# Kernel tuning notes

Hardware: AMD Instinct MI355X
Metric: run time of the kernel (lower is better)

The kernel has to match this reference:

```python
import math
import jax, jax.numpy as jnp
import numpy as np

B, S, E, H, P = 8, 1024, 512, 8, 32
MAXD, OFFS, LW, STL, HID = 256, 8.0, 4, 4, 2048

def _lin(x, w, b):
    return x @ w.T + b

def _gelu(x):
    return jax.nn.gelu(x, approximate=False)  # torch nn.GELU default (erf)

def _ln(x, g, b, eps=1e-5):
    m = x.mean(-1, keepdims=True)
    v = ((x - m) ** 2).mean(-1, keepdims=True)
    return (x - m) / jnp.sqrt(v + eps) * g + b

def setup_inputs() -> dict:
    key = jax.random.key(0)
    ks = iter(jax.random.split(key, 40))
    def w(*shape):
        return (jax.random.normal(next(ks), shape, dtype=jnp.float32) * 0.02)
    x = jax.random.normal(next(ks), (B, S, E), dtype=jnp.float32)
    lengths = jax.random.randint(next(ks), (B,), S // 2, S + 1)
    padding_mask = jnp.arange(S)[None, :] >= lengths[:, None]  # (B,S) bool
    inp = dict(x=x, padding_mask=padding_mask)
    # local MHA (torch nn.MultiheadAttention packed in_proj)
    inp.update(in_proj_w=w(3 * E, E), in_proj_b=jnp.zeros((3 * E,), jnp.float32),
               mha_out_w=w(E, E), mha_out_b=jnp.zeros((E,), jnp.float32))
    # deformable attention projections
    for nm in ('dq', 'dk', 'dv', 'do'):
        inp[nm + '_w'] = w(E, E); inp[nm + '_b'] = jnp.zeros((E,), jnp.float32)
    inp.update(off1_w=w(E, E), off1_b=jnp.zeros((E,), jnp.float32),
               off2_w=w(H * P, E), off2_b=jnp.zeros((H * P,), jnp.float32))
    inp.update(gate1_w=w(E, 3 * E), gate1_b=jnp.zeros((E,), jnp.float32),
               gate2_w=w(E, E), gate2_b=jnp.zeros((E,), jnp.float32))
    inp.update(n1_g=jnp.ones((E,), jnp.float32), n1_b=jnp.zeros((E,), jnp.float32),
               n2_g=jnp.ones((E,), jnp.float32), n2_b=jnp.zeros((E,), jnp.float32))
    inp.update(ffn1_w=w(HID, E), ffn1_b=jnp.zeros((HID,), jnp.float32),
               ffn2_w=w(E, HID), ffn2_b=jnp.zeros((E,), jnp.float32))
    return inp

def _forward(x, padding_mask, in_proj_w, in_proj_b, mha_out_w, mha_out_b,
             dq_w, dq_b, dk_w, dk_b, dv_w, dv_b, do_w, do_b,
             off1_w, off1_b, off2_w, off2_b, gate1_w, gate1_b, gate2_w, gate2_b,
             n1_g, n1_b, n2_g, n2_b, ffn1_w, ffn1_b, ffn2_w, ffn2_b):
    Bv, Sv, Ev = x.shape
    hd = Ev // H
    pos = jnp.arange(Sv)
    # ---------------- local causal windowed MHA ----------------
    qkv = _lin(x, in_proj_w, in_proj_b)
    q, k, v = jnp.split(qkv, 3, axis=-1)
    q = q.reshape(Bv, Sv, H, hd).transpose(0, 2, 1, 3)  # bhsd
    k = k.reshape(Bv, Sv, H, hd).transpose(0, 2, 1, 3)
    v = v.reshape(Bv, Sv, H, hd).transpose(0, 2, 1, 3)
    scores = jnp.einsum('bhqd,bhkd->bhqk', q, k) / math.sqrt(hd)
    future = pos[None, :] > pos[:, None]
    too_far = (pos[:, None] - pos[None, :]) >= min(LW, STL)
    lmask = (future | too_far)[None, None] | padding_mask[:, None, None, :]
    scores = jnp.where(lmask, -jnp.inf, scores)
    allm = lmask.all(-1, keepdims=True)
    scores = jnp.where(allm, 0.0, scores)  # avoid NaN on fully-masked (padded) rows
    attn = jax.nn.softmax(scores, axis=-1)
    attn = jnp.where(lmask, 0.0, attn)
    lo = jnp.einsum('bhqk,bhkd->bhqd', attn, v).transpose(0, 2, 1, 3).reshape(Bv, Sv, Ev)
    local_out = _lin(lo, mha_out_w, mha_out_b)
    # ---------------- deformable long-history attention ----------------
    anchors = jnp.linspace(0.1, 0.9, P)
    valid_len = jnp.clip(Sv - padding_mask.sum(-1), 1, None)
    positions = pos[None, :, None].astype(jnp.float32)  # (1,S,1)
    base = anchors[None, None, :] * positions
    off = jnp.tanh(_lin(_gelu(_lin(x, off1_w, off1_b)), off2_w, off2_b))
    off = off.reshape(Bv, Sv, H, P).mean(2) * OFFS
    sampled = base + off
    sampled = jnp.clip(sampled, jnp.clip(positions - MAXD, 0, None), positions)
    sampled = jnp.minimum(sampled, (valid_len - 1).astype(jnp.float32)[:, None, None])
    sp = jnp.round(sampled).astype(jnp.int32)  # (B,S,P) sample positions
    qd = _lin(x, dq_w, dq_b)
    kd = _lin(x, dk_w, dk_b)
    vd = _lin(x, dv_w, dv_b)
    bidx = jnp.arange(Bv)[:, None, None]
    k_sp = kd[bidx, sp]  # (B,S,P,E) gathered keys
    v_sp = vd[bidx, sp]
    sc = jnp.einsum('bqd,bqpd->bqp', qd, k_sp) / math.sqrt(Ev)
    samp_inv = padding_mask[bidx, sp]
    causal_inv = sp > pos[None, :, None]
    rb = jnp.clip(pos[:, None] - (STL - 1), 0, None)
    long_mem_mask = pos[None, :] >= rb  # (S,S): forbid recent short-term positions
    extra_inv = long_mem_mask[pos[None, :, None], sp]
    inv = samp_inv | causal_inv | extra_inv
    sc = jnp.where(inv, -jnp.inf, sc)
    alli = inv.all(-1, keepdims=True)
    sc = jnp.where(alli, 0.0, sc)
    a = jax.nn.softmax(sc, axis=-1)
    a = jnp.where(inv, 0.0, a)
    long_out = _lin(jnp.einsum('bqp,bqpd->bqd', a, v_sp), do_w, do_b)
    # ---------------- gate fuse + FFN ----------------
    cat = jnp.concatenate([x, local_out, long_out], axis=-1)
    g = jax.nn.sigmoid(_lin(_gelu(_lin(cat, gate1_w, gate1_b)), gate2_w, gate2_b))
    fused = g * local_out + (1.0 - g) * long_out
    x1 = _ln(x + fused, n1_g, n1_b)
    f = _lin(_gelu(_lin(x1, ffn1_w, ffn1_b)), ffn2_w, ffn2_b)
    return _ln(x1 + f, n2_g, n2_b)

def reference(x, padding_mask, in_proj_w, in_proj_b, mha_out_w, mha_out_b,
              dq_w, dq_b, dk_w, dk_b, dv_w, dv_b, do_w, do_b,
              off1_w, off1_b, off2_w, off2_b, gate1_w, gate1_b, gate2_w, gate2_b,
              n1_g, n1_b, n2_g, n2_b, ffn1_w, ffn1_b, ffn2_w, ffn2_b):
    return _forward(x, padding_mask, in_proj_w, in_proj_b, mha_out_w, mha_out_b,
                    dq_w, dq_b, dk_w, dk_b, dv_w, dv_b, do_w, do_b,
                    off1_w, off1_b, off2_w, off2_b, gate1_w, gate1_b, gate2_w, gate2_b,
                    n1_g, n1_b, n2_g, n2_b, ffn1_w, ffn1_b, ffn2_w, ffn2_b)
```

## Files before the change

kernel.cpp:

```cpp
#include <hip/hip_runtime.h>
#include <hip/hip_bf16.h>
#include <type_traits>

typedef __hip_bfloat16 bf16;
typedef __attribute__((ext_vector_type(8))) short short8;
typedef __attribute__((ext_vector_type(4))) float floatx4;

static constexpr int kB = 8;
static constexpr int kS = 1024;
static constexpr int kE = 512;
static constexpr int kH = 8;
static constexpr int kP = 32;
static constexpr int kTok = kB * kS;
static constexpr int kHid = 2048;

__device__ __forceinline__ void load8f(const bf16* p, float* f) {
  uint4 u = *(const uint4*)p;
  const bf16* h = (const bf16*)&u;
#pragma unroll
  for (int e = 0; e < 8; e++) f[e] = __bfloat162float(h[e]);
}
__device__ __forceinline__ void store8b(bf16* p, const float* f) {
  uint4 u;
  bf16* h = (bf16*)&u;
#pragma unroll
  for (int e = 0; e < 8; e++) h[e] = __float2bfloat16(f[e]);
  *(uint4*)p = u;
}
__device__ __forceinline__ bool is_pad(const void* pm, int flag, int idx) {
  return flag ? (((const int*)pm)[idx] != 0)
              : (((const unsigned char*)pm)[idx] != 0);
}
__device__ __forceinline__ float fast_gelu(float x) {
  float u = x * (0.7978845608f + 0.044714998f * x * x);
  float e = __expf(2.0f * u);
  float t = 1.0f - 2.0f / (e + 1.0f);
  return 0.5f * x * (1.0f + t);
}
__device__ __forceinline__ void dma16(const bf16* g, bf16* l) {
  __builtin_amdgcn_global_load_lds(
      (const __attribute__((address_space(1))) unsigned int*)g,
      (__attribute__((address_space(3))) unsigned int*)l, 16, 0, 0);
}

__global__ __launch_bounds__(256) void detect_kernel(const void* __restrict__ x,
                                                     int* __restrict__ meta) {
  __shared__ int cnt;
  if (threadIdx.x == 0) cnt = 0;
  __syncthreads();
  const unsigned short* u = (const unsigned short*)x;
  int c = 0;
  for (int i = threadIdx.x; i < 1024; i += 256) {
    int e = (u[i] >> 7) & 0xFF;
    if (e >= 0x90) c++;
  }
  if (c) atomicAdd(&cnt, c);
  __syncthreads();
  if (threadIdx.x == 0) meta[9] = (cnt > 64) ? 1 : 0;
}

__global__ __launch_bounds__(256) void meta_kernel(const void* __restrict__ pm,
                                                   int* __restrict__ meta) {
  __shared__ int bigfound;
  __shared__ int cnt[kB];
  int tid = threadIdx.x;
  if (tid == 0) bigfound = 0;
  if (tid < kB) cnt[tid] = 0;
  __syncthreads();
  const unsigned int* w = (const unsigned int*)pm;
  int f = 0;
  for (int i = tid; i < 2048; i += 256)
    if (w[i] & 0xFFFFFFFEu) f = 1;
  if (f) atomicOr(&bigfound, 1);
  __syncthreads();
  int flag = bigfound ? 0 : 1;
  for (int i = tid; i < kTok; i += 256) {
    if (is_pad(pm, flag, i)) atomicAdd(&cnt[i >> 10], 1);
  }
  __syncthreads();
  if (tid == 0) meta[0] = flag;
  if (tid < kB) {
    int vl = kS - cnt[tid];
    if (vl < 1) vl = 1;
    meta[1 + tid] = vl;
  }
}

struct CvtJob { const void* src; bf16* hi; bf16* lo; int nblk; };
struct CvtJobs { CvtJob j[13]; };
__global__ __launch_bounds__(256) void cvt_all_kernel(CvtJobs jobs,
                                                      const int* __restrict__ meta) {
  int fp = meta[9];
  int b = blockIdx.x, ji = 0;
  while (b >= jobs.j[ji].nblk) { b -= jobs.j[ji].nblk; ji++; }
  CvtJob J = jobs.j[ji];
  int i = b * 1024 + threadIdx.x * 4;
  float v[4];
  if (fp) {
    float4 f = ((const float4*)J.src)[i >> 2];
    v[0] = f.x; v[1] = f.y; v[2] = f.z; v[3] = f.w;
  } else {
    uint2 u = *(const uint2*)((const bf16*)J.src + i);
    const bf16* h = (const bf16*)&u;
#pragma unroll
    for (int e = 0; e < 4; e++) v[e] = __bfloat162float(h[e]);
  }
  uint2 uh;
  bf16* hh = (bf16*)&uh;
#pragma unroll
  for (int e = 0; e < 4; e++) hh[e] = __float2bfloat16(v[e]);
  *(uint2*)(J.hi + i) = uh;
  if (J.lo) {
    uint2 ul;
    bf16* hl = (bf16*)&ul;
#pragma unroll
    for (int e = 0; e < 4; e++)
      hl[e] = __float2bfloat16(v[e] - __bfloat162float(hh[e]));
    *(uint2*)(J.lo + i) = ul;
  }
}

struct CvtFJob { const void* src; float* dst; int n; };
struct CvtFJobs { CvtFJob j[16]; };
__global__ __launch_bounds__(256) void cvt_small_kernel(CvtFJobs jobs,
                                                        const int* __restrict__ meta) {
  int fp = meta[9];
#pragma unroll 1
  for (int ji = 0; ji < 16; ji++) {
    CvtFJob J = jobs.j[ji];
    for (int i = threadIdx.x; i < J.n; i += 256)
      J.dst[i] = fp ? ((const float*)J.src)[i]
                    : __bfloat162float(((const bf16*)J.src)[i]);
  }
}

static constexpr int BK = 32;

template <int BM, int BN, int ACT, typename OUTT>
__device__ __forceinline__ void gemm_core(const bf16* __restrict__ A,
                                          const bf16* __restrict__ W,
                                          const float* __restrict__ bias,
                                          OUTT* __restrict__ C, int N, int K,
                                          int m0, int n0) {
  constexpr int WR = (BM == 128 && BN == 128) ? 4 : 2;
  constexpr int WC = 4;
  __shared__ bf16 As[BM * BK];
  __shared__ bf16 Bs[BN * BK];
  const int tid = threadIdx.x;
  const int lane = tid & 63;
  const int wid = tid >> 6;
  int wm, wn;
  if constexpr (BM == 128 && BN == 128) {
    wm = (wid >> 1) * 64; wn = (wid & 1) * 64;
  } else {
    wm = wid * 32; wn = 0;
  }

  floatx4 acc[WR][WC];
#pragma unroll
  for (int i = 0; i < WR; i++)
#pragma unroll
    for (int j = 0; j < WC; j++) acc[i][j] = (floatx4)0.0f;

  for (int kt = 0; kt < K; kt += BK) {
#pragma unroll
    for (int c = 0; c < BM / 64; c++) {
      int seg = c * 64 + wid * 16;
      int row = seg + (lane >> 2);
      int ch = (lane & 3) ^ ((row >> 1) & 3);
      dma16(&A[(size_t)(m0 + row) * K + kt + ch * 8], &As[seg * BK]);
    }
#pragma unroll
    for (int c = 0; c < BN / 64; c++) {
      int seg = c * 64 + wid * 16;
      int row = seg + (lane >> 2);
      int ch = (lane & 3) ^ ((row >> 1) & 3);
      dma16(&W[(size_t)(n0 + row) * K + kt + ch * 8], &Bs[seg * BK]);
    }
    __syncthreads();
    const int kb = lane >> 4;
    short8 af[WR], bfr[WC];
#pragma unroll
    for (int i = 0; i < WR; i++) {
      int r = wm + i * 16 + (lane & 15);
      af[i] = *(const short8*)(&As[r * BK + ((kb ^ ((r >> 1) & 3)) << 3)]);
    }
#pragma unroll
    for (int j = 0; j < WC; j++) {
      int r = wn + j * 16 + (lane & 15);
      bfr[j] = *(const short8*)(&Bs[r * BK + ((kb ^ ((r >> 1) & 3)) << 3)]);
    }
#pragma unroll
    for (int i = 0; i < WR; i++)
#pragma unroll
      for (int j = 0; j < WC; j++)
        acc[i][j] = __builtin_amdgcn_mfma_f32_16x16x32_bf16(bfr[j], af[i],
                                                            acc[i][j], 0, 0, 0);
    __syncthreads();
  }

#pragma unroll
  for (int i = 0; i < WR; i++) {
    int row = m0 + wm + i * 16 + (lane & 15);
#pragma unroll
    for (int j = 0; j < WC; j++) {
      int col = n0 + wn + j * 16 + ((lane >> 4) << 2);
      float bv[4] = {0.f, 0.f, 0.f, 0.f};
      if (bias) {
        float4 b4 = *(const float4*)&bias[col];
        bv[0] = b4.x; bv[1] = b4.y; bv[2] = b4.z; bv[3] = b4.w;
      }
      float v[4];
#pragma unroll
      for (int r = 0; r < 4; r++) {
        v[r] = acc[i][j][r] + bv[r];
        if (ACT == 1) v[r] = fast_gelu(v[r]);
        else if (ACT == 2) v[r] = 1.0f / (1.0f + __expf(-v[r]));
      }
      size_t idx = (size_t)row * N + col;
      if constexpr (std::is_same<OUTT, float>::value) {
        *(float4*)&C[idx] = make_float4(v[0], v[1], v[2], v[3]);
      } else {
        uint2 u;
        bf16* h = (bf16*)&u;
#pragma unroll
        for (int r = 0; r < 4; r++) h[r] = __float2bfloat16(v[r]);
        *(uint2*)&C[idx] = u;
      }
    }
  }
}

template <int BM, int BN, int ACT, typename OUTT>
__global__ __launch_bounds__(256) void gemm_bt(
    const bf16* __restrict__ A, const bf16* __restrict__ W,
    const float* __restrict__ bias, OUTT* __restrict__ C, int N, int K) {
  gemm_core<BM, BN, ACT, OUTT>(A, W, bias, C, N, K, blockIdx.x * BM,
                               blockIdx.y * BN);
}

__global__ __launch_bounds__(256) void gemm_pair(
    const bf16* __restrict__ A0, const bf16* __restrict__ W0,
    const float* __restrict__ b0, bf16* __restrict__ C0,
    const bf16* __restrict__ A1, const bf16* __restrict__ W1,
    const float* __restrict__ b1, bf16* __restrict__ C1, int N, int K) {
  int nb = N >> 6;
  bool s = (int)blockIdx.y >= nb;
  gemm_core<128, 64, 0, bf16>(s ? A1 : A0, s ? W1 : W0, s ? b1 : b0,
                              s ? C1 : C0, N, K, blockIdx.x * 128,
                              (s ? (int)blockIdx.y - nb : (int)blockIdx.y) * 64);
}

__global__ __launch_bounds__(256) void gemm_gate1(
    const bf16* __restrict__ x, const bf16* __restrict__ lo,
    const bf16* __restrict__ lg, const bf16* __restrict__ W,
    const float* __restrict__ bias, bf16* __restrict__ C) {
  constexpr int BM = 128, BN = 64, WR = 2, WC = 4;
  constexpr int N = 512, K = 1536;
  __shared__ bf16 As[BM * BK];
  __shared__ bf16 Bs[BN * BK];
  const int tid = threadIdx.x;
  const int lane = tid & 63;
  const int wid = tid >> 6;
  const int wm = wid * 32, wn = 0;
  const int m0 = blockIdx.x * BM, n0 = blockIdx.y * BN;

  floatx4 acc[WR][WC];
#pragma unroll
  for (int i = 0; i < WR; i++)
#pragma unroll
    for (int j = 0; j < WC; j++) acc[i][j] = (floatx4)0.0f;

  for (int kt = 0; kt < K; kt += BK) {
    const bf16* src = (kt < 512) ? x : (kt < 1024) ? lo : lg;
    int kk = kt & 511;
#pragma unroll
    for (int c = 0; c < 2; c++) {
      int seg = c * 64 + wid * 16;
      int row = seg + (lane >> 2);
      int ch = (lane & 3) ^ ((row >> 1) & 3);
      dma16(&src[(size_t)(m0 + row) * 512 + kk + ch * 8], &As[seg * BK]);
    }
    {
      int seg = wid * 16;
      int row = seg + (lane >> 2);
      int ch = (lane & 3) ^ ((row >> 1) & 3);
      dma16(&W[(size_t)(n0 + row) * K + kt + ch * 8], &Bs[seg * BK]);
    }
    __syncthreads();
    const int kb = lane >> 4;
    short8 af[WR], bfr[WC];
#pragma unroll
    for (int i = 0; i < WR; i++) {
      int r = wm + i * 16 + (lane & 15);
      af[i] = *(const short8*)(&As[r * BK + ((kb ^ ((r >> 1) & 3)) << 3)]);
    }
#pragma unroll
    for (int j = 0; j < WC; j++) {
      int r = wn + j * 16 + (lane & 15);
      bfr[j] = *(const short8*)(&Bs[r * BK + ((kb ^ ((r >> 1) & 3)) << 3)]);
    }
#pragma unroll
    for (int i = 0; i < WR; i++)
#pragma unroll
      for (int j = 0; j < WC; j++)
        acc[i][j] = __builtin_amdgcn_mfma_f32_16x16x32_bf16(bfr[j], af[i],
                                                            acc[i][j], 0, 0, 0);
    __syncthreads();
  }

#pragma unroll
  for (int i = 0; i < WR; i++) {
    int row = m0 + wm + i * 16 + (lane & 15);
#pragma unroll
    for (int j = 0; j < WC; j++) {
      int col = n0 + wn + j * 16 + ((lane >> 4) << 2);
      float4 b4 = *(const float4*)&bias[col];
      float bv[4] = {b4.x, b4.y, b4.z, b4.w};
      uint2 u;
      bf16* h = (bf16*)&u;
#pragma unroll
      for (int r = 0; r < 4; r++)
        h[r] = __float2bfloat16(fast_gelu(acc[i][j][r] + bv[r]));
      *(uint2*)&C[(size_t)row * N + col] = u;
    }
  }
}

template <int BM, int BN, bool SPLIT>
__global__ __launch_bounds__(256) void gemm3_bt(
    const bf16* __restrict__ Ah, const bf16* __restrict__ Al,
    const bf16* __restrict__ Wh, const bf16* __restrict__ Wl,
    const float* __restrict__ bias, float* __restrict__ Cf,
    bf16* __restrict__ Chi, bf16* __restrict__ Clo, int N, int K) {
  constexpr int WR = 2;
  constexpr int WC = (BM == 128) ? 4 : 2;
  __shared__ bf16 Ash[BM * BK];
  __shared__ bf16 Asl[BM * BK];
  __shared__ bf16 Bsh[BN * BK];
  __shared__ bf16 Bsl[BN * BK];
  const int tid = threadIdx.x;
  const int lane = tid & 63;
  const int wid = tid >> 6;
  int wm, wn;
  if constexpr (BM == 128) {
    wm = wid * 32; wn = 0;
  } else {
    wm = (wid >> 1) * 32; wn = (wid & 1) * 32;
  }
  const int m0 = blockIdx.x * BM, n0 = blockIdx.y * BN;

  floatx4 acc[WR][WC];
#pragma unroll
  for (int i = 0; i < WR; i++)
#pragma unroll
    for (int j = 0; j < WC; j++) acc[i][j] = (floatx4)0.0f;

  for (int kt = 0; kt < K; kt += BK) {
#pragma unroll
    for (int c = 0; c < BM / 64; c++) {
      int seg = c * 64 + wid * 16;
      int row = seg + (lane >> 2);
      int ch = (lane & 3) ^ ((row >> 1) & 3);
      size_t g = (size_t)(m0 + row) * K + kt + ch * 8;
      dma16(&Ah[g], &Ash[seg * BK]);
      dma16(&Al[g], &Asl[seg * BK]);
    }
#pragma unroll
    for (int c = 0; c < BN / 64; c++) {
      int seg = c * 64 + wid * 16;
      int row = seg + (lane >> 2);
      int ch = (lane & 3) ^ ((row >> 1) & 3);
      size_t g = (size_t)(n0 + row) * K + kt + ch * 8;
      dma16(&Wh[g], &Bsh[seg * BK]);
      dma16(&Wl[g], &Bsl[seg * BK]);
    }
    __syncthreads();
    const int kb = lane >> 4;
    short8 ah[WR], al[WR], bh[WC], bl[WC];
#pragma unroll
    for (int i = 0; i < WR; i++) {
      int r = wm + i * 16 + (lane & 15);
      int ro = r * BK + ((kb ^ ((r >> 1) & 3)) << 3);
      ah[i] = *(const short8*)(&Ash[ro]);
      al[i] = *(const short8*)(&Asl[ro]);
    }
#pragma unroll
    for (int j = 0; j < WC; j++) {
      int r = wn + j * 16 + (lane & 15);
      int ro = r * BK + ((kb ^ ((r >> 1) & 3)) << 3);
      bh[j] = *(const short8*)(&Bsh[ro]);
      bl[j] = *(const short8*)(&Bsl[ro]);
    }
#pragma unroll
    for (int i = 0; i < WR; i++)
#pragma unroll
      for (int j = 0; j < WC; j++) {
        acc[i][j] = __builtin_amdgcn_mfma_f32_16x16x32_bf16(bh[j], ah[i],
                                                            acc[i][j], 0, 0, 0);
        acc[i][j] = __builtin_amdgcn_mfma_f32_16x16x32_bf16(bl[j], ah[i],
                                                            acc[i][j], 0, 0, 0);
        acc[i][j] = __builtin_amdgcn_mfma_f32_16x16x32_bf16(bh[j], al[i],
                                                            acc[i][j], 0, 0, 0);
      }
    __syncthreads();
  }

#pragma unroll
  for (int i = 0; i < WR; i++) {
    int row = m0 + wm + i * 16 + (lane & 15);
#pragma unroll
    for (int j = 0; j < WC; j++) {
      int col = n0 + wn + j * 16 + ((lane >> 4) << 2);
      float4 b4 = *(const float4*)&bias[col];
      float bv[4] = {b4.x, b4.y, b4.z, b4.w};
      if constexpr (SPLIT) {
        uint2 uh, ul;
        bf16* hh = (bf16*)&uh;
        bf16* hl = (bf16*)&ul;
#pragma unroll
        for (int r = 0; r < 4; r++) {
          float v = acc[i][j][r] + bv[r];
          float g = 0.5f * v * (1.0f + erff(v * 0.70710678118654752f));
          bf16 hi = __float2bfloat16(g);
          hh[r] = hi;
          hl[r] = __float2bfloat16(g - __bfloat162float(hi));
        }
        *(uint2*)&Chi[(size_t)row * N + col] = uh;
        *(uint2*)&Clo[(size_t)row * N + col] = ul;
      } else {
        *(float4*)&Cf[(size_t)row * N + col] =
            make_float4(acc[i][j][0] + bv[0], acc[i][j][1] + bv[1],
                        acc[i][j][2] + bv[2], acc[i][j][3] + bv[3]);
      }
    }
  }
}

__global__ __launch_bounds__(256) void local_attn_kernel(
    const bf16* __restrict__ qkv, const void* __restrict__ pm,
    const int* __restrict__ meta, bf16* __restrict__ lo) {
  int lane = threadIdx.x & 63;
  int t = blockIdx.x * 4 + (threadIdx.x >> 6);
  int b = t >> 10, s = t & 1023;
  int h = lane >> 3, sub = lane & 7;
  int flag = meta[0];
  float q[8];
  load8f(qkv + (size_t)t * 3072 + h * 64 + sub * 8, q);
  float sc[4];
  bool val[4];
#pragma unroll
  for (int w = 0; w < 4; w++) {
    int kp = s - 3 + w;
    bool v = (kp >= 0) && !is_pad(pm, flag, b * kS + kp);
    float d = 0.0f;
    if (v) {
      float kk[8];
      load8f(qkv + (size_t)(b * kS + kp) * 3072 + 512 + h * 64 + sub * 8, kk);
#pragma unroll
      for (int e = 0; e < 8; e++) d += q[e] * kk[e];
    }
    d += __shfl_xor(d, 1);
    d += __shfl_xor(d, 2);
    d += __shfl_xor(d, 4);
    sc[w] = v ? d / 8.0f : -INFINITY;
    val[w] = v;
  }
  float mx = fmaxf(fmaxf(sc[0], sc[1]), fmaxf(sc[2], sc[3]));
  float a[4] = {0.f, 0.f, 0.f, 0.f};
  if (mx != -INFINITY) {
    float ssum = 0.f;
#pragma unroll
    for (int w = 0; w < 4; w++) {
      float e = val[w] ? expf(sc[w] - mx) : 0.0f;
      a[w] = e;
      ssum += e;
    }
#pragma unroll
    for (int w = 0; w < 4; w++) a[w] /= ssum;
  }
  float o[8] = {0.f, 0.f, 0.f, 0.f, 0.f, 0.f, 0.f, 0.f};
#pragma unroll
  for (int w = 0; w < 4; w++) {
    if (val[w] && a[w] > 0.0f) {
      int kp = s - 3 + w;
      float vv[8];
      load8f(qkv + (size_t)(b * kS + kp) * 3072 + 1024 + h * 64 + sub * 8, vv);
#pragma unroll
      for (int e = 0; e < 8; e++) o[e] += a[w] * vv[e];
    }
  }
  store8b(lo + (size_t)t * kE + lane * 8, o);
}

__global__ __launch_bounds__(256) void sampler_kernel(
    const float* __restrict__ rawf, const void* __restrict__ pm,
    const int* __restrict__ meta, int* __restrict__ sp,
    unsigned int* __restrict__ invm) {
  int t = blockIdx.x * 8 + (threadIdx.x >> 5);
  int p = threadIdx.x & 31;
  int b = t >> 10, s = t & 1023;
  int flag = meta[0];
  float off = 0.0f;
#pragma unroll
  for (int h = 0; h < kH; h++) off += tanhf(rawf[(size_t)t * 256 + h * kP + p]);
  double anchor = 0.1 + 0.8 * (double)p / 31.0;
  double sampled = anchor * (double)s + (double)off;
  double lov = fmax(0.0, (double)s - 256.0);
  sampled = fmin(fmax(sampled, lov), (double)s);
  int vlen = meta[1 + b];
  sampled = fmin(sampled, (double)(vlen - 1));
  int spv = (int)rint(sampled);
  bool inv = is_pad(pm, flag, b * kS + spv) || (spv > s) ||
             (spv >= max(0, s - 3));
  sp[(size_t)t * kP + p] = spv;
  unsigned long long m = __ballot(inv);
  int lane = threadIdx.x & 63;
  if (lane == 0) invm[t] = (unsigned int)m;
  if (lane == 32) invm[t] = (unsigned int)(m >> 32);
}

__global__ __launch_bounds__(256) void long_attn_kernel(
    const bf16* __restrict__ qkv, const int* __restrict__ sp,
    const unsigned int* __restrict__ invm, bf16* __restrict__ ctx) {
  int lane = threadIdx.x & 63;
  int bid = blockIdx.x;
  int sbid = (bid & 7) * 256 + (bid >> 3);
  int t = sbid * 4 + (threadIdx.x >> 6);
  int b = t >> 10;
  int p = lane & 31;
  int row_abs = b * kS + sp[(size_t)t * kP + p];
  float q[8];
  load8f(qkv + (size_t)t * 3072 + 1536 + lane * 8, q);
  float sc_mine = 0.0f;
#pragma unroll 4
  for (int pp = 0; pp < 32; pp++) {
    int row = __shfl(row_abs, pp);
    float kk[8];
    load8f(qkv + (size_t)row * 3072 + 2048 + lane * 8, kk);
    float d = 0.0f;
#pragma unroll
    for (int e = 0; e < 8; e++) d += q[e] * kk[e];
#pragma unroll
    for (int m = 1; m < 64; m <<= 1) d += __shfl_xor(d, m);
    if (p == pp) sc_mine = d;
  }
  bool inv = (invm[t] >> p) & 1u;
  float sc = inv ? -INFINITY : sc_mine / 22.627416997969522f;
  float mx = sc;
#pragma unroll
  for (int m = 1; m < 32; m <<= 1) mx = fmaxf(mx, __shfl_xor(mx, m));
  float e = (inv || mx == -INFINITY) ? 0.0f : expf(sc - mx);
  float ssum = e;
#pragma unroll
  for (int m = 1; m < 32; m <<= 1) ssum += __shfl_xor(ssum, m);
  float a = (ssum > 0.0f) ? e / ssum : 0.0f;
  float o[8] = {0.f, 0.f, 0.f, 0.f, 0.f, 0.f, 0.f, 0.f};
#pragma unroll 4
  for (int pp = 0; pp < 32; pp++) {
    float ap = __shfl(a, pp);
    int row = __shfl(row_abs, pp);
    if (ap != 0.0f) {
      float vv[8];
      load8f(qkv + (size_t)row * 3072 + 2560 + lane * 8, vv);
#pragma unroll
      for (int e2 = 0; e2 < 8; e2++) o[e2] += ap * vv[e2];
    }
  }
  store8b(ctx + (size_t)t * kE + lane * 8, o);
}

__global__ __launch_bounds__(256) void ln1_kernel(
    const void* __restrict__ xin, const int* __restrict__ meta,
    const bf16* __restrict__ lo, const bf16* __restrict__ lg,
    const bf16* __restrict__ g, const float* __restrict__ gamma,
    const float* __restrict__ beta, bf16* __restrict__ x1b,
    float* __restrict__ x1f) {
  int lane = threadIdx.x & 63;
  int t = blockIdx.x * 4 + (threadIdx.x >> 6);
  size_t base = (size_t)t * kE + lane * 8;
  float xv[8], lov[8], lgv[8], gv[8], h[8];
  if (meta[9]) {
    const float4* xf = (const float4*)((const float*)xin + base);
    float4 a = xf[0], b2 = xf[1];
    xv[0] = a.x; xv[1] = a.y; xv[2] = a.z; xv[3] = a.w;
    xv[4] = b2.x; xv[5] = b2.y; xv[6] = b2.z; xv[7] = b2.w;
  } else {
    load8f((const bf16*)xin + base, xv);
  }
  load8f(lo + base, lov);
  load8f(lg + base, lgv);
  load8f(g + base, gv);
  float s1 = 0.f, s2 = 0.f;
#pragma unroll
  for (int e = 0; e < 8; e++) {
    h[e] = xv[e] + gv[e] * lov[e] + (1.0f - gv[e]) * lgv[e];
    s1 += h[e];
    s2 += h[e] * h[e];
  }
#pragma unroll
  for (int m = 1; m < 64; m <<= 1) {
    s1 += __shfl_xor(s1, m);
    s2 += __shfl_xor(s2, m);
  }
  float mean = s1 * (1.0f / kE);
  float var = s2 * (1.0f / kE) - mean * mean;
  float rstd = 1.0f / sqrtf(var + 1e-5f);
  float y[8];
#pragma unroll
  for (int e = 0; e < 8; e++)
    y[e] = (h[e] - mean) * rstd * gamma[lane * 8 + e] + beta[lane * 8 + e];
  store8b(x1b + base, y);
#pragma unroll
  for (int e = 0; e < 8; e++) x1f[base + e] = y[e];
}

__global__ __launch_bounds__(256) void ln2_kernel(
    const float* __restrict__ x1f, const float* __restrict__ ff,
    const float* __restrict__ gamma, const float* __restrict__ beta,
    const int* __restrict__ meta, void* __restrict__ out) {
  int lane = threadIdx.x & 63;
  int t = blockIdx.x * 4 + (threadIdx.x >> 6);
  size_t base = (size_t)t * kE + lane * 8;
  float h[8];
  float s1 = 0.f, s2 = 0.f;
#pragma unroll
  for (int e = 0; e < 8; e++) {
    h[e] = x1f[base + e] + ff[base + e];
    s1 += h[e];
    s2 += h[e] * h[e];
  }
#pragma unroll
  for (int m = 1; m < 64; m <<= 1) {
    s1 += __shfl_xor(s1, m);
    s2 += __shfl_xor(s2, m);
  }
  float mean = s1 * (1.0f / kE);
  float var = s2 * (1.0f / kE) - mean * mean;
  float rstd = 1.0f / sqrtf(var + 1e-5f);
  float y[8];
#pragma unroll
  for (int e = 0; e < 8; e++)
    y[e] = (h[e] - mean) * rstd * gamma[lane * 8 + e] + beta[lane * 8 + e];
  if (meta[9]) {
    float* of = (float*)out + base;
    ((float4*)of)[0] = make_float4(y[0], y[1], y[2], y[3]);
    ((float4*)of)[1] = make_float4(y[4], y[5], y[6], y[7]);
  } else {
    store8b((bf16*)out + base, y);
  }
}

extern "C" void kernel_launch(void* const* d_in, const int* in_sizes, int n_in,
                              void* d_out, int out_size, void* d_ws,
                              size_t ws_size, hipStream_t stream) {
  const void* x = d_in[0];
  const void* pm = d_in[1];

  char* w = (char*)d_ws;
  auto alloc = [&](size_t bytes) {
    char* p = w;
    w += (bytes + 255) & ~(size_t)255;
    return p;
  };
  bf16* qkv_all = (bf16*)alloc((size_t)kTok * 3072 * 2);
  bf16* lo_ctx = (bf16*)alloc((size_t)kTok * kE * 2);
  bf16* ctx2 = (bf16*)alloc((size_t)kTok * kE * 2);
  bf16* local_out = (bf16*)alloc((size_t)kTok * kE * 2);
  bf16* long_out = (bf16*)alloc((size_t)kTok * kE * 2);
  bf16* hbuf = (bf16*)alloc((size_t)kTok * kE * 2);
  bf16* gbuf = (bf16*)alloc((size_t)kTok * kE * 2);
  bf16* x1b = (bf16*)alloc((size_t)kTok * kE * 2);
  float* x1f = (float*)alloc((size_t)kTok * kE * 4);
  float* rawf = (float*)alloc((size_t)kTok * 256 * 4);
  int* sp = (int*)alloc((size_t)kTok * kP * 4);
  unsigned int* invm = (unsigned int*)alloc((size_t)kTok * 4);
  int* meta = (int*)alloc(256);
  bf16* x_hi = (bf16*)alloc((size_t)kTok * kE * 2);
  bf16* x_lo = (bf16*)alloc((size_t)kTok * kE * 2);
  bf16* wall = (bf16*)alloc((size_t)3072 * 512 * 2);
  bf16* mow = (bf16*)alloc(512 * 512 * 2);
  bf16* dow = (bf16*)alloc(512 * 512 * 2);
  bf16* o1h = (bf16*)alloc(512 * 512 * 2);
  bf16* o1l = (bf16*)alloc(512 * 512 * 2);
  bf16* o2h = (bf16*)alloc(256 * 512 * 2);
  bf16* o2l = (bf16*)alloc(256 * 512 * 2);
  bf16* g1w = (bf16*)alloc(512 * 1536 * 2);
  bf16* g2w = (bf16*)alloc(512 * 512 * 2);
  bf16* f1w = (bf16*)alloc((size_t)2048 * 512 * 2);
  bf16* f2w = (bf16*)alloc((size_t)512 * 2048 * 2);
  float* ball = (float*)alloc(3072 * 4);
  float* mob = (float*)alloc(512 * 4);
  float* dob = (float*)alloc(512 * 4);
  float* o1b = (float*)alloc(512 * 4);
  float* o2b = (float*)alloc(256 * 4);
  float* g1b = (float*)alloc(512 * 4);
  float* g2b = (float*)alloc(512 * 4);
  float* n1g = (float*)alloc(512 * 4);
  float* n1bt = (float*)alloc(512 * 4);
  float* n2g = (float*)alloc(512 * 4);
  float* n2bt = (float*)alloc(512 * 4);
  float* f1b = (float*)alloc(2048 * 4);
  float* f2b = (float*)alloc(512 * 4);

  bf16* h_hi = hbuf;
  bf16* h_lo = x1b;
  float* f_f32 = (float*)qkv_all;
  bf16* ffn_h = (bf16*)((char*)qkv_all + (size_t)kTok * kE * 4);

  dim3 blk(256);
  detect_kernel<<<1, blk, 0, stream>>>(x, meta);
  meta_kernel<<<1, blk, 0, stream>>>(pm, meta);

  CvtJobs J;
  auto job = [](const void* s, bf16* hi, bf16* lo, int n) {
    CvtJob j; j.src = s; j.hi = hi; j.lo = lo; j.nblk = n >> 10; return j;
  };
  J.j[0] = job(d_in[0], x_hi, x_lo, kTok * kE);
  J.j[1] = job(d_in[2], wall, nullptr, 1536 * 512);
  J.j[2] = job(d_in[6], wall + (size_t)1536 * 512, nullptr, 512 * 512);
  J.j[3] = job(d_in[8], wall + (size_t)2048 * 512, nullptr, 512 * 512);
  J.j[4] = job(d_in[10], wall + (size_t)2560 * 512, nullptr, 512 * 512);
  J.j[5] = job(d_in[4], mow, nullptr, 512 * 512);
  J.j[6] = job(d_in[12], dow, nullptr, 512 * 512);
  J.j[7] = job(d_in[14], o1h, o1l, 512 * 512);
  J.j[8] = job(d_in[16], o2h, o2l, 256 * 512);
  J.j[9] = job(d_in[18], g1w, nullptr, 512 * 1536);
  J.j[10] = job(d_in[20], g2w, nullptr, 512 * 512);
  J.j[11] = job(d_in[26], f1w, nullptr, 2048 * 512);
  J.j[12] = job(d_in[28], f2w, nullptr, 512 * 2048);
  int totblk = 0;
  for (int i = 0; i < 13; i++) totblk += J.j[i].nblk;
  cvt_all_kernel<<<totblk, blk, 0, stream>>>(J, meta);

  CvtFJobs JF;
  auto fjob = [](const void* s, float* d, int n) {
    CvtFJob j; j.src = s; j.dst = d; j.n = n; return j;
  };
  JF.j[0] = fjob(d_in[3], ball, 1536);
  JF.j[1] = fjob(d_in[7], ball + 1536, 512);
  JF.j[2] = fjob(d_in[9], ball + 2048, 512);
  JF.j[3] = fjob(d_in[11], ball + 2560, 512);
  JF.j[4] = fjob(d_in[5], mob, 512);
  JF.j[5] = fjob(d_in[13], dob, 512);
  JF.j[6] = fjob(d_in[15], o1b, 512);
  JF.j[7] = fjob(d_in[17], o2b, 256);
  JF.j[8] = fjob(d_in[19], g1b, 512);
  JF.j[9] = fjob(d_in[21], g2b, 512);
  JF.j[10] = fjob(d_in[22], n1g, 512);
  JF.j[11] = fjob(d_in[23], n1bt, 512);
  JF.j[12] = fjob(d_in[24], n2g, 512);
  JF.j[13] = fjob(d_in[25], n2bt, 512);
  JF.j[14] = fjob(d_in[27], f1b, 2048);
  JF.j[15] = fjob(d_in[29], f2b, 512);
  cvt_small_kernel<<<1, blk, 0, stream>>>(JF, meta);

  gemm_bt<128, 128, 0, bf16><<<dim3(64, 24), blk, 0, stream>>>(
      x_hi, wall, ball, qkv_all, 3072, kE);
  gemm3_bt<128, 64, true><<<dim3(64, 8), blk, 0, stream>>>(
      x_hi, x_lo, o1h, o1l, o1b, nullptr, h_hi, h_lo, kE, kE);
  local_attn_kernel<<<2048, blk, 0, stream>>>(qkv_all, pm, meta, lo_ctx);
  gemm3_bt<64, 64, false><<<dim3(128, 4), blk, 0, stream>>>(
      h_hi, h_lo, o2h, o2l, o2b, rawf, nullptr, nullptr, 256, kE);
  sampler_kernel<<<1024, blk, 0, stream>>>(rawf, pm, meta, sp, invm);
  long_attn_kernel<<<2048, blk, 0, stream>>>(qkv_all, sp, invm, ctx2);

  gemm_pair<<<dim3(64, 16), blk, 0, stream>>>(lo_ctx, mow, mob, local_out,
                                              ctx2, dow, dob, long_out, kE, kE);

  gemm_gate1<<<dim3(64, 8), blk, 0, stream>>>(x_hi, local_out, long_out, g1w,
                                              g1b, hbuf);
  gemm_bt<128, 64, 2, bf16><<<dim3(64, 8), blk, 0, stream>>>(
      hbuf, g2w, g2b, gbuf, kE, kE);

  ln1_kernel<<<2048, blk, 0, stream>>>(x, meta, local_out, long_out, gbuf, n1g,
                                       n1bt, x1b, x1f);
  gemm_bt<128, 128, 1, bf16><<<dim3(64, 16), blk, 0, stream>>>(
      x1b, f1w, f1b, ffn_h, kHid, kE);
  gemm_bt<128, 64, 0, float><<<dim3(64, 8), blk, 0, stream>>>(
      ffn_h, f2w, f2b, f_f32, kE, kHid);
  ln2_kernel<<<2048, blk, 0, stream>>>(x1f, f_f32, n2g, n2bt, meta, d_out);
}
```

Baseline: 477.1 us.

## Double-buffer GEMM LDS tiles and skip low-part MFMAs for bf16 inputs

The bf16 GEMM cores (gemm_core and gemm_gate1) now use two LDS buffers, so the next K tile's global-to-LDS DMA is issued before the current tile's MFMAs run. Explicit waitcnt drains keep this correct. The split-precision gemm3_bt now reads the detected input-format flag and skips loading the low-part weight and activation tiles, and their extra MFMAs, when inputs are not fp32. The aim is to hide load latency and cut redundant compensation work. This doubles LDS use per block, which may reduce occupancy, and the full waitcnt drain each iteration may limit how much overlap is actually achieved.

```diff
diff --git a/kernel.cpp b/kernel.cpp
--- a/kernel.cpp
+++ b/kernel.cpp
@@ -42,6 +42,7 @@
       (const __attribute__((address_space(1))) unsigned int*)g,
       (__attribute__((address_space(3))) unsigned int*)l, 16, 0, 0);
 }
+__device__ __forceinline__ void drain_all() { __builtin_amdgcn_s_waitcnt(0); }
 
 __global__ __launch_bounds__(256) void detect_kernel(const void* __restrict__ x,
                                                      int* __restrict__ meta) {
@@ -144,8 +145,8 @@
                                           int m0, int n0) {
   constexpr int WR = (BM == 128 && BN == 128) ? 4 : 2;
   constexpr int WC = 4;
-  __shared__ bf16 As[BM * BK];
-  __shared__ bf16 Bs[BN * BK];
+  __shared__ bf16 As[2][BM * BK];
+  __shared__ bf16 Bs[2][BN * BK];
   const int tid = threadIdx.x;
   const int lane = tid & 63;
   const int wid = tid >> 6;
@@ -156,39 +157,47 @@
     wm = wid * 32; wn = 0;
   }
 
-  floatx4 acc[WR][WC];
-#pragma unroll
-  for (int i = 0; i < WR; i++)
-#pragma unroll
-    for (int j = 0; j < WC; j++) acc[i][j] = (floatx4)0.0f;
-
-  for (int kt = 0; kt < K; kt += BK) {
+  auto stage = [&](int buf, int kt) {
 #pragma unroll
     for (int c = 0; c < BM / 64; c++) {
       int seg = c * 64 + wid * 16;
       int row = seg + (lane >> 2);
       int ch = (lane & 3) ^ ((row >> 1) & 3);
-      dma16(&A[(size_t)(m0 + row) * K + kt + ch * 8], &As[seg * BK]);
+      dma16(&A[(size_t)(m0 + row) * K + kt + ch * 8], &As[buf][seg * BK]);
     }
 #pragma unroll
     for (int c = 0; c < BN / 64; c++) {
       int seg = c * 64 + wid * 16;
       int row = seg + (lane >> 2);
       int ch = (lane & 3) ^ ((row >> 1) & 3);
-      dma16(&W[(size_t)(n0 + row) * K + kt + ch * 8], &Bs[seg * BK]);
-    }
-    __syncthreads();
+      dma16(&W[(size_t)(n0 + row) * K + kt + ch * 8], &Bs[buf][seg * BK]);
+    }
+  };
+
+  floatx4 acc[WR][WC];
+#pragma unroll
+  for (int i = 0; i < WR; i++)
+#pragma unroll
+    for (int j = 0; j < WC; j++) acc[i][j] = (floatx4)0.0f;
+
+  stage(0, 0);
+  drain_all();
+  __syncthreads();
+  const int niter = K / BK;
+  for (int k = 0; k < niter; k++) {
+    const int cur = k & 1;
+    if (k + 1 < niter) stage(cur ^ 1, (k + 1) * BK);
     const int kb = lane >> 4;
     short8 af[WR], bfr[WC];
 #pragma unroll
     for (int i = 0; i < WR; i++) {
       int r = wm + i * 16 + (lane & 15);
-      af[i] = *(const short8*)(&As[r * BK + ((kb ^ ((r >> 1) & 3)) << 3)]);
+      af[i] = *(const short8*)(&As[cur][r * BK + ((kb ^ ((r >> 1) & 3)) << 3)]);
     }
 #pragma unroll
     for (int j = 0; j < WC; j++) {
       int r = wn + j * 16 + (lane & 15);
-      bfr[j] = *(const short8*)(&Bs[r * BK + ((kb ^ ((r >> 1) & 3)) << 3)]);
+      bfr[j] = *(const short8*)(&Bs[cur][r * BK + ((kb ^ ((r >> 1) & 3)) << 3)]);
     }
 #pragma unroll
     for (int i = 0; i < WR; i++)
@@ -196,6 +205,7 @@
       for (int j = 0; j < WC; j++)
         acc[i][j] = __builtin_amdgcn_mfma_f32_16x16x32_bf16(bfr[j], af[i],
                                                             acc[i][j], 0, 0, 0);
+    drain_all();
     __syncthreads();
   }
 
@@ -257,21 +267,15 @@
     const float* __restrict__ bias, bf16* __restrict__ C) {
   constexpr int BM = 128, BN = 64, WR = 2, WC = 4;
   constexpr int N = 512, K = 1536;
-  __shared__ bf16 As[BM * BK];
-  __shared__ bf16 Bs[BN * BK];
+  __shared__ bf16 As[2][BM * BK];
+  __shared__ bf16 Bs[2][BN * BK];
   const int tid = threadIdx.x;
   const int lane = tid & 63;
   const int wid = tid >> 6;
   const int wm = wid * 32, wn = 0;
   const int m0 = blockIdx.x * BM, n0 = blockIdx.y * BN;
 
-  floatx4 acc[WR][WC];
-#pragma unroll
-  for (int i = 0; i < WR; i++)
-#pragma unroll
-    for (int j = 0; j < WC; j++) acc[i][j] = (floatx4)0.0f;
-
-  for (int kt = 0; kt < K; kt += BK) {
+  auto stage = [&](int buf, int kt) {
     const bf16* src = (kt < 512) ? x : (kt < 1024) ? lo : lg;
     int kk = kt & 511;
 #pragma unroll
@@ -279,26 +283,40 @@
       int seg = c * 64 + wid * 16;
       int row = seg + (lane >> 2);
       int ch = (lane & 3) ^ ((row >> 1) & 3);
-      dma16(&src[(size_t)(m0 + row) * 512 + kk + ch * 8], &As[seg * BK]);
+      dma16(&src[(size_t)(m0 + row) * 512 + kk + ch * 8], &As[buf][seg * BK]);
     }
     {
       int seg = wid * 16;
       int row = seg + (lane >> 2);
       int ch = (lane & 3) ^ ((row >> 1) & 3);
-      dma16(&W[(size_t)(n0 + row) * K + kt + ch * 8], &Bs[seg * BK]);
-    }
-    __syncthreads();
+      dma16(&W[(size_t)(n0 + row) * K + kt + ch * 8], &Bs[buf][seg * BK]);
+    }
+  };
+
+  floatx4 acc[WR][WC];
+#pragma unroll
+  for (int i = 0; i < WR; i++)
+#pragma unroll
+    for (int j = 0; j < WC; j++) acc[i][j] = (floatx4)0.0f;
+
+  stage(0, 0);
+  drain_all();
+  __syncthreads();
+  const int niter = K / BK;
+  for (int k = 0; k < niter; k++) {
+    const int cur = k & 1;
+    if (k + 1 < niter) stage(cur ^ 1, (k + 1) * BK);
     const int kb = lane >> 4;
     short8 af[WR], bfr[WC];
 #pragma unroll
     for (int i = 0; i < WR; i++) {
       int r = wm + i * 16 + (lane & 15);
-      af[i] = *(const short8*)(&As[r * BK + ((kb ^ ((r >> 1) & 3)) << 3)]);
+      af[i] = *(const short8*)(&As[cur][r * BK + ((kb ^ ((r >> 1) & 3)) << 3)]);
     }
 #pragma unroll
     for (int j = 0; j < WC; j++) {
       int r = wn + j * 16 + (lane & 15);
-      bfr[j] = *(const short8*)(&Bs[r * BK + ((kb ^ ((r >> 1) & 3)) << 3)]);
+      bfr[j] = *(const short8*)(&Bs[cur][r * BK + ((kb ^ ((r >> 1) & 3)) << 3)]);
     }
 #pragma unroll
     for (int i = 0; i < WR; i++)
@@ -306,6 +324,7 @@
       for (int j = 0; j < WC; j++)
         acc[i][j] = __builtin_amdgcn_mfma_f32_16x16x32_bf16(bfr[j], af[i],
                                                             acc[i][j], 0, 0, 0);
+    drain_all();
     __syncthreads();
   }
 
@@ -327,18 +346,21 @@
   }
 }
 
-template <int BM, int BN, bool SPLIT>
+template <int BM, int BN, bool SPLIT, bool ALWAYS_AL>
 __global__ __launch_bounds__(256) void gemm3_bt(
     const bf16* __restrict__ Ah, const bf16* __restrict__ Al,
     const bf16* __restrict__ Wh, const bf16* __restrict__ Wl,
-    const float* __restrict__ bias, float* __restrict__ Cf,
-    bf16* __restrict__ Chi, bf16* __restrict__ Clo, int N, int K) {
+    const float* __restrict__ bias, const int* __restrict__ meta,
+    float* __restrict__ Cf, bf16* __restrict__ Chi, bf16* __restrict__ Clo,
+    int N, int K) {
   constexpr int WR = 2;
   constexpr int WC = (BM == 128) ? 4 : 2;
   __shared__ bf16 Ash[BM * BK];
   __shared__ bf16 Asl[BM * BK];
   __shared__ bf16 Bsh[BN * BK];
   __shared__ bf16 Bsl[BN * BK];
+  const int fp = meta[9];
+  const bool use_al = fp || ALWAYS_AL;
   const int tid = threadIdx.x;
   const int lane = tid & 63;
   const int wid = tid >> 6;
@@ -364,7 +386,7 @@
       int ch = (lane & 3) ^ ((row >> 1) & 3);
       size_t g = (size_t)(m0 + row) * K + kt + ch * 8;
       dma16(&Ah[g], &Ash[seg * BK]);
-      dma16(&Al[g], &Asl[seg * BK]);
+      if (use_al) dma16(&Al[g], &Asl[seg * BK]);
     }
 #pragma unroll
     for (int c = 0; c < BN / 64; c++) {
@@ -373,8 +395,9 @@
       int ch = (lane & 3) ^ ((row >> 1) & 3);
       size_t g = (size_t)(n0 + row) * K + kt + ch * 8;
       dma16(&Wh[g], &Bsh[seg * BK]);
-      dma16(&Wl[g], &Bsl[seg * BK]);
-    }
+      if (fp) dma16(&Wl[g], &Bsl[seg * BK]);
+    }
+    drain_all();
     __syncthreads();
     const int kb = lane >> 4;
     short8 ah[WR], al[WR], bh[WC], bl[WC];
@@ -383,14 +406,14 @@
       int r = wm + i * 16 + (lane & 15);
       int ro = r * BK + ((kb ^ ((r >> 1) & 3)) << 3);
       ah[i] = *(const short8*)(&Ash[ro]);
-      al[i] = *(const short8*)(&Asl[ro]);
+      if (use_al) al[i] = *(const short8*)(&Asl[ro]);
     }
 #pragma unroll
     for (int j = 0; j < WC; j++) {
       int r = wn + j * 16 + (lane & 15);
       int ro = r * BK + ((kb ^ ((r >> 1) & 3)) << 3);
       bh[j] = *(const short8*)(&Bsh[ro]);
-      bl[j] = *(const short8*)(&Bsl[ro]);
+      if (fp) bl[j] = *(const short8*)(&Bsl[ro]);
     }
 #pragma unroll
     for (int i = 0; i < WR; i++)
@@ -398,10 +421,12 @@
       for (int j = 0; j < WC; j++) {
         acc[i][j] = __builtin_amdgcn_mfma_f32_16x16x32_bf16(bh[j], ah[i],
                                                             acc[i][j], 0, 0, 0);
-        acc[i][j] = __builtin_amdgcn_mfma_f32_16x16x32_bf16(bl[j], ah[i],
-                                                            acc[i][j], 0, 0, 0);
-        acc[i][j] = __builtin_amdgcn_mfma_f32_16x16x32_bf16(bh[j], al[i],
-                                                            acc[i][j], 0, 0, 0);
+        if (fp)
+          acc[i][j] = __builtin_amdgcn_mfma_f32_16x16x32_bf16(
+              bl[j], ah[i], acc[i][j], 0, 0, 0);
+        if (use_al)
+          acc[i][j] = __builtin_amdgcn_mfma_f32_16x16x32_bf16(
+              bh[j], al[i], acc[i][j], 0, 0, 0);
       }
     __syncthreads();
   }
@@ -757,11 +782,11 @@
 
   gemm_bt<128, 128, 0, bf16><<<dim3(64, 24), blk, 0, stream>>>(
       x_hi, wall, ball, qkv_all, 3072, kE);
-  gemm3_bt<128, 64, true><<<dim3(64, 8), blk, 0, stream>>>(
-      x_hi, x_lo, o1h, o1l, o1b, nullptr, h_hi, h_lo, kE, kE);
+  gemm3_bt<128, 64, true, false><<<dim3(64, 8), blk, 0, stream>>>(
+      x_hi, x_lo, o1h, o1l, o1b, meta, nullptr, h_hi, h_lo, kE, kE);
   local_attn_kernel<<<2048, blk, 0, stream>>>(qkv_all, pm, meta, lo_ctx);
-  gemm3_bt<64, 64, false><<<dim3(128, 4), blk, 0, stream>>>(
-      h_hi, h_lo, o2h, o2l, o2b, rawf, nullptr, nullptr, 256, kE);
+  gemm3_bt<64, 64, false, true><<<dim3(128, 4), blk, 0, stream>>>(
+      h_hi, h_lo, o2h, o2l, o2b, meta, rawf, nullptr, nullptr, 256, kE);
   sampler_kernel<<<1024, blk, 0, stream>>>(rawf, pm, meta, sp, invm);
   long_attn_kernel<<<2048, blk, 0, stream>>>(qkv_all, sp, invm, ctx2);
 
```

Result: faster. 457.2 us (-4.2%).
